# Performance work log

Measured on AMD Instinct MI355X. Metric: run time of the kernel, lower is better.

Reference implementation:

```python
import jax, jax.numpy as jnp
import numpy as np

EPS = 1e-08
SLOPE = 0.01  # LeakyReLU default negative_slope
B = 2097152
H = 32

def leaky_relu(x):
    return jnp.where(x >= 0, x, SLOPE * x)

def gram_schmidt(v, w):
    # v, w: [b,3]
    v_on = v / (jnp.linalg.norm(v, axis=-1, keepdims=True) + EPS)
    proj = jnp.sum(w * v_on, axis=-1, keepdims=True) * v_on
    w_orth = w - proj
    w_on = w_orth / (jnp.linalg.norm(w_orth, axis=-1, keepdims=True) + EPS)
    u_on = jnp.cross(v_on, w_on)
    R = jnp.stack((v_on, w_on, u_on), axis=-1)  # [b,3,3]
    v_local = jnp.einsum('bji,bj->bi', R, v)    # R^T @ v
    w_local = jnp.einsum('bji,bj->bi', R, w)
    return R, v_local, w_local

def setup_inputs() -> dict:
    key = jax.random.key(0)
    ks = jax.random.split(key, 12)
    std = 0.0001  # init_weights() normal std
    return {
        'v': jax.random.normal(ks[0], (B, 3), jnp.float32),
        'w': jax.random.normal(ks[1], (B, 3), jnp.float32),
        'W1': jax.random.normal(ks[2], (H, 3), jnp.float32) * std,
        'b1': jax.random.normal(ks[3], (H,), jnp.float32) * std,
        'W2': jax.random.normal(ks[4], (H, H), jnp.float32) * std,
        'b2': jax.random.normal(ks[5], (H,), jnp.float32) * std,
        'Wd1': jax.random.normal(ks[6], (H, H), jnp.float32) * std,
        'bd1': jax.random.normal(ks[7], (H,), jnp.float32) * std,
        'Wd2': jax.random.normal(ks[8], (3, H), jnp.float32) * std,
        'bd2': jax.random.normal(ks[9], (3,), jnp.float32) * std,
        'bias': jnp.array([[0.0, 0.0, -9.81]], jnp.float32),
    }

def reference(v, w, W1, b1, W2, b2, Wd1, bd1, Wd2, bd2, bias):
    shapes = v.shape
    b = shapes[0]
    v = v.reshape(b, 3)
    w = w.reshape(b, 3)
    R, v_local, w_local = gram_schmidt(v, w)
    feat = jnp.concatenate([v_local[..., :1], w_local[..., :2]], axis=-1)  # [b,3]
    h1 = leaky_relu(feat @ W1.T + b1)           # [b,H]
    h = leaky_relu(h1 @ W2.T + b2) * h1         # [b,H]
    y = leaky_relu(h @ Wd1.T + bd1) @ Wd2.T + bd2  # [b,3]
    y = jnp.einsum('bij,bj->bi', R, y) + bias
    return y.reshape(shapes)
```

## Files before the change

kernel.cpp:

```cpp
#include <hip/hip_runtime.h>

typedef __attribute__((ext_vector_type(8))) short short8;
typedef __attribute__((ext_vector_type(4))) float f32x4;
typedef __attribute__((ext_vector_type(2))) float f32x2;
typedef __attribute__((ext_vector_type(4))) unsigned int u32x4;

static __device__ __forceinline__ unsigned int fbits(float f) {
    union { float f; unsigned int u; } v; v.f = f; return v.u;
}
static __device__ __forceinline__ float bitsf(unsigned int u) {
    union { float f; unsigned int u; } v; v.u = u; return v.f;
}
static __device__ __forceinline__ unsigned int pkbf(float lo, float hi) {
    return __builtin_amdgcn_perm(fbits(hi), fbits(lo), 0x07060302u);
}
static __device__ __forceinline__ float bflo(unsigned int u) { return bitsf(u << 16); }
static __device__ __forceinline__ float bfhi(unsigned int u) { return bitsf(u & 0xFFFF0000u); }
static __device__ __forceinline__ float leaky(float x) { return fmaxf(x, 0.01f * x); }
static __device__ __forceinline__ float rsqrt_nr(float x) {
    const float r = __builtin_amdgcn_rsqf(x);
    return r * (1.5f - (0.5f * x) * (r * r));
}
static __device__ __forceinline__ f32x2 pk_mul_s(f32x2 s, f32x2 v) {
    f32x2 d; asm("v_pk_mul_f32 %0, %1, %2" : "=v"(d) : "s"(s), "v"(v)); return d;
}
static __device__ __forceinline__ f32x2 pk_fma_s(f32x2 s, f32x2 v, f32x2 c) {
    f32x2 d; asm("v_pk_fma_f32 %0, %1, %2, %3" : "=v"(d) : "s"(s), "v"(v), "v"(c)); return d;
}
static __device__ __forceinline__ f32x2 pk_add_s(f32x2 s, f32x2 v) {
    f32x2 d; asm("v_pk_add_f32 %0, %1, %2" : "=v"(d) : "s"(s), "v"(v)); return d;
}
static __device__ __forceinline__ f32x2 pk_mul_v(f32x2 a, f32x2 b) {
    f32x2 d; asm("v_pk_mul_f32 %0, %1, %2" : "=v"(d) : "v"(a), "v"(b)); return d;
}
static __device__ __forceinline__ f32x2 pk_fma_v(f32x2 a, f32x2 b, f32x2 c) {
    f32x2 d; asm("v_pk_fma_f32 %0, %1, %2, %3" : "=v"(d) : "v"(a), "v"(b), "v"(c)); return d;
}
static __device__ __forceinline__ f32x2 leaky2(f32x2 x, f32x2 c001) {
    const f32x2 m = pk_mul_v(x, c001);
    f32x2 r; r.x = fmaxf(x.x, m.x); r.y = fmaxf(x.y, m.y); return r;
}


__global__ __launch_bounds__(256, 4) void aero_mfma(
    const float* __restrict__ vin, const float* __restrict__ win,
    const float* __restrict__ gW1, const float* __restrict__ gb1,
    const float* __restrict__ gW2, const float* __restrict__ gb2,
    const float* __restrict__ gWd1, const float* __restrict__ gbd1,
    const float* __restrict__ gWd2, const float* __restrict__ gbd2,
    const float* __restrict__ gbias,
    float* __restrict__ out, int nrows)
{
    __shared__ unsigned int h1lds[256 * 20];

    const int tid  = threadIdx.x;
    int row = blockIdx.x * 256 + tid;
    if (row >= nrows) row = nrows - 1;

    const int i15   = tid & 15;
    const int quad  = (tid >> 4) & 3;
    const int wbase = tid & 192;
    const int ko    = 4 * quad;

    unsigned int aW2lo[4], aW2hi[4], aWd1lo[4], aWd1hi[4];
    {
        const float* p;
        p = gW2 + i15 * 32 + ko;
        { f32x4 xa = *(const f32x4*)p, xb = *(const f32x4*)(p + 16);
          #pragma unroll
          for (int j = 0; j < 4; ++j) aW2lo[j] = pkbf(xa[j], xb[j]); }
        p = gW2 + (16 + i15) * 32 + ko;
        { f32x4 xa = *(const f32x4*)p, xb = *(const f32x4*)(p + 16);
          #pragma unroll
          for (int j = 0; j < 4; ++j) aW2hi[j] = pkbf(xa[j], xb[j]); }
        p = gWd1 + i15 * 32 + ko;
        { f32x4 xa = *(const f32x4*)p, xb = *(const f32x4*)(p + 16);
          #pragma unroll
          for (int j = 0; j < 4; ++j) aWd1lo[j] = pkbf(xa[j], xb[j]); }
        p = gWd1 + (16 + i15) * 32 + ko;
        { f32x4 xa = *(const f32x4*)p, xb = *(const f32x4*)(p + 16);
          #pragma unroll
          for (int j = 0; j < 4; ++j) aWd1hi[j] = pkbf(xa[j], xb[j]); }
    }
    f32x2 wd2p[3][4];
    #pragma unroll
    for (int f = 0; f < 3; ++f) {
        const f32x4 xa = *(const f32x4*)(gWd2 + f * 32 + ko);
        const f32x4 xb = *(const f32x4*)(gWd2 + f * 32 + ko + 16);
        #pragma unroll
        for (int r = 0; r < 4; ++r) { wd2p[f][r].x = xa[r]; wd2p[f][r].y = xb[r]; }
    }
    const f32x4 cb2lo  = *(const f32x4*)(gb2  + ko);
    const f32x4 cb2hi  = *(const f32x4*)(gb2  + 16 + ko);
    const f32x4 cbd1lo = *(const f32x4*)(gbd1 + ko);
    const f32x4 cbd1hi = *(const f32x4*)(gbd1 + 16 + ko);

    const float v0 = vin[3 * row + 0], v1 = vin[3 * row + 1], v2 = vin[3 * row + 2];
    const float w0 = win[3 * row + 0], w1 = win[3 * row + 1], w2 = win[3 * row + 2];

    const float sv  = v0 * v0 + v1 * v1 + v2 * v2;
    const float rnv = rsqrt_nr(sv);
    const float a0 = v0 * rnv, a1 = v1 * rnv, a2 = v2 * rnv;
    const float proj = w0 * a0 + w1 * a1 + w2 * a2;
    const float o0 = w0 - proj * a0, o1 = w1 - proj * a1, o2 = w2 - proj * a2;
    const float sw  = o0 * o0 + o1 * o1 + o2 * o2;
    const float rnw = rsqrt_nr(sw);
    const float c0 = o0 * rnw, c1 = o1 * rnw, c2 = o2 * rnw;
    const float u0 = a1 * c2 - a2 * c1;
    const float u1 = a2 * c0 - a0 * c2;
    const float u2 = a0 * c1 - a1 * c0;

    const float f0 = sv * rnv, f1 = proj, f2 = sw * rnw;

    const f32x2 c001 = {0.01f, 0.01f};
    {
        const f32x2 fv0 = {f0, f0}, fv1 = {f1, f1}, fv2 = {f2, f2};
        unsigned int hp[16];
        #pragma unroll
        for (int j = 0; j < 16; ++j) {
            const f32x2 wp0 = {gW1[3 * j + 0], gW1[3 * (j + 16) + 0]};
            const f32x2 wp1 = {gW1[3 * j + 1], gW1[3 * (j + 16) + 1]};
            const f32x2 wp2 = {gW1[3 * j + 2], gW1[3 * (j + 16) + 2]};
            const f32x2 bb  = {gb1[j], gb1[j + 16]};
            f32x2 acc = pk_mul_s(wp0, fv0);
            acc = pk_fma_s(wp1, fv1, acc);
            acc = pk_fma_s(wp2, fv2, acc);
            acc = pk_add_s(bb, acc);
            const f32x2 h = leaky2(acc, c001);
            hp[j] = pkbf(h.x, h.y);
        }
        unsigned int* dst = &h1lds[tid * 20];
        *(u32x4*)(dst +  0) = (u32x4){hp[0],  hp[1],  hp[2],  hp[3]};
        *(u32x4*)(dst +  4) = (u32x4){hp[4],  hp[5],  hp[6],  hp[7]};
        *(u32x4*)(dst +  8) = (u32x4){hp[8],  hp[9],  hp[10], hp[11]};
        *(u32x4*)(dst + 12) = (u32x4){hp[12], hp[13], hp[14], hp[15]};
    }
    __syncthreads();

    float y0 = 0.f, y1 = 0.f, y2 = 0.f;
    #pragma unroll
    for (int t = 0; t < 4; ++t) {
        const u32x4 bfr = *(const u32x4*)(&h1lds[(wbase + 16 * t + i15) * 20 + ko]);
        const short8 bfrag = __builtin_bit_cast(short8, bfr);

        const f32x4 accA = __builtin_amdgcn_mfma_f32_16x16x32_bf16(
            __builtin_bit_cast(short8, (u32x4){aW2lo[0], aW2lo[1], aW2lo[2], aW2lo[3]}),
            bfrag, cb2lo, 0, 0, 0);
        const f32x4 accB = __builtin_amdgcn_mfma_f32_16x16x32_bf16(
            __builtin_bit_cast(short8, (u32x4){aW2hi[0], aW2hi[1], aW2hi[2], aW2hi[3]}),
            bfrag, cb2hi, 0, 0, 0);

        u32x4 h2u;
        #pragma unroll
        for (int r = 0; r < 4; ++r)
            h2u[r] = pkbf(leaky(accA[r]) * bflo(bfr[r]),
                          leaky(accB[r]) * bfhi(bfr[r]));
        const short8 h2frag = __builtin_bit_cast(short8, h2u);

        const f32x4 accC = __builtin_amdgcn_mfma_f32_16x16x32_bf16(
            __builtin_bit_cast(short8, (u32x4){aWd1lo[0], aWd1lo[1], aWd1lo[2], aWd1lo[3]}),
            h2frag, cbd1lo, 0, 0, 0);
        const f32x4 accD = __builtin_amdgcn_mfma_f32_16x16x32_bf16(
            __builtin_bit_cast(short8, (u32x4){aWd1hi[0], aWd1hi[1], aWd1hi[2], aWd1hi[3]}),
            h2frag, cbd1hi, 0, 0, 0);

        f32x2 h3p[4];
        #pragma unroll
        for (int r = 0; r < 4; ++r) { h3p[r].x = leaky(accC[r]); h3p[r].y = leaky(accD[r]); }
        f32x2 P0 = pk_mul_v(wd2p[0][0], h3p[0]);
        f32x2 P1 = pk_mul_v(wd2p[1][0], h3p[0]);
        f32x2 P2 = pk_mul_v(wd2p[2][0], h3p[0]);
        #pragma unroll
        for (int r = 1; r < 4; ++r) {
            P0 = pk_fma_v(wd2p[0][r], h3p[r], P0);
            P1 = pk_fma_v(wd2p[1][r], h3p[r], P1);
            P2 = pk_fma_v(wd2p[2][r], h3p[r], P2);
        }
        float s0 = P0.x + P0.y, s1 = P1.x + P1.y, s2 = P2.x + P2.y;
        s0 += __shfl_xor(s0, 16); s0 += __shfl_xor(s0, 32);
        s1 += __shfl_xor(s1, 16); s1 += __shfl_xor(s1, 32);
        s2 += __shfl_xor(s2, 16); s2 += __shfl_xor(s2, 32);
        if (quad == t) { y0 = s0; y1 = s1; y2 = s2; }
    }
    y0 += gbd2[0]; y1 += gbd2[1]; y2 += gbd2[2];

    out[3 * row + 0] = fmaf(a0, y0, fmaf(c0, y1, fmaf(u0, y2, gbias[0])));
    out[3 * row + 1] = fmaf(a1, y0, fmaf(c1, y1, fmaf(u1, y2, gbias[1])));
    out[3 * row + 2] = fmaf(a2, y0, fmaf(c2, y1, fmaf(u2, y2, gbias[2])));
}

extern "C" void kernel_launch(void* const* d_in, const int* in_sizes, int n_in,
                              void* d_out, int out_size, void* d_ws, size_t ws_size,
                              hipStream_t stream) {
    const float* v    = (const float*)d_in[0];
    const float* w    = (const float*)d_in[1];
    const float* W1   = (const float*)d_in[2];
    const float* b1   = (const float*)d_in[3];
    const float* W2   = (const float*)d_in[4];
    const float* b2   = (const float*)d_in[5];
    const float* Wd1  = (const float*)d_in[6];
    const float* bd1  = (const float*)d_in[7];
    const float* Wd2  = (const float*)d_in[8];
    const float* bd2  = (const float*)d_in[9];
    const float* bias = (const float*)d_in[10];

    const int nrows = in_sizes[0] / 3;
    dim3 block(256);
    dim3 grid((nrows + 255) / 256);
    hipLaunchKernelGGL(aero_mfma, grid, block, 0, stream,
                       v, w, W1, b1, W2, b2, Wd1, bd1, Wd2, bd2, bias,
                       (float*)d_out, nrows);
}
```

Baseline: 140.5 us.

## Process two rows per thread to amortize weight fragment setup

Each block now handles 512 rows with 256 threads, so each thread runs the Gram-Schmidt and first layer for two rows and then runs the MFMA chain twice. Per-thread weight loading, bf16 packing and constant setup are spread over twice as many rows, and the grid is halved. The cost is double the LDS per block and higher register pressure, which could reduce occupancy under the 4-block launch bound.

```diff
diff --git a/kernel.cpp b/kernel.cpp
--- a/kernel.cpp
+++ b/kernel.cpp
@@ -41,6 +41,96 @@
     f32x2 r; r.x = fmaxf(x.x, m.x); r.y = fmaxf(x.y, m.y); return r;
 }
 
+
+struct Rot { float a0,a1,a2,c0,c1,c2,u0,u1,u2; };
+
+static __device__ __forceinline__ Rot gs_l1(
+    const float* __restrict__ vin, const float* __restrict__ win,
+    const float* __restrict__ gW1, const float* __restrict__ gb1,
+    int row, unsigned int* __restrict__ dst)
+{
+    const float v0 = vin[3*row+0], v1 = vin[3*row+1], v2 = vin[3*row+2];
+    const float w0 = win[3*row+0], w1 = win[3*row+1], w2 = win[3*row+2];
+    const float sv  = v0*v0 + v1*v1 + v2*v2;
+    const float rnv = rsqrt_nr(sv);
+    const float a0 = v0*rnv, a1 = v1*rnv, a2 = v2*rnv;
+    const float proj = w0*a0 + w1*a1 + w2*a2;
+    const float o0 = w0 - proj*a0, o1 = w1 - proj*a1, o2 = w2 - proj*a2;
+    const float sw  = o0*o0 + o1*o1 + o2*o2;
+    const float rnw = rsqrt_nr(sw);
+    const float c0 = o0*rnw, c1 = o1*rnw, c2 = o2*rnw;
+    const float u0 = a1*c2 - a2*c1;
+    const float u1 = a2*c0 - a0*c2;
+    const float u2 = a0*c1 - a1*c0;
+    const float f0 = sv*rnv, f1 = proj, f2 = sw*rnw;
+
+    const f32x2 c001 = {0.01f, 0.01f};
+    const f32x2 fv0 = {f0,f0}, fv1 = {f1,f1}, fv2 = {f2,f2};
+    unsigned int hp[16];
+    #pragma unroll
+    for (int j = 0; j < 16; ++j) {
+        const f32x2 wp0 = {gW1[3*j+0], gW1[3*(j+16)+0]};
+        const f32x2 wp1 = {gW1[3*j+1], gW1[3*(j+16)+1]};
+        const f32x2 wp2 = {gW1[3*j+2], gW1[3*(j+16)+2]};
+        const f32x2 bb  = {gb1[j], gb1[j+16]};
+        f32x2 acc = pk_mul_s(wp0, fv0);
+        acc = pk_fma_s(wp1, fv1, acc);
+        acc = pk_fma_s(wp2, fv2, acc);
+        acc = pk_add_s(bb, acc);
+        const f32x2 h = leaky2(acc, c001);
+        hp[j] = pkbf(h.x, h.y);
+    }
+    *(u32x4*)(dst+0)  = (u32x4){hp[0],hp[1],hp[2],hp[3]};
+    *(u32x4*)(dst+4)  = (u32x4){hp[4],hp[5],hp[6],hp[7]};
+    *(u32x4*)(dst+8)  = (u32x4){hp[8],hp[9],hp[10],hp[11]};
+    *(u32x4*)(dst+12) = (u32x4){hp[12],hp[13],hp[14],hp[15]};
+    return {a0,a1,a2,c0,c1,c2,u0,u1,u2};
+}
+
+#define CHAIN234(LB, Y0, Y1, Y2)                                                   \
+    {                                                                              \
+        float s0k = 0.f, s1k = 0.f, s2k = 0.f;                                     \
+        _Pragma("unroll")                                                          \
+        for (int t = 0; t < 4; ++t) {                                              \
+            const u32x4 bfr = *(const u32x4*)(                                     \
+                &h1lds[((LB) + wbase + 16*t + i15)*20 + ko]);                      \
+            const short8 bfrag = __builtin_bit_cast(short8, bfr);                  \
+            const f32x4 accA = __builtin_amdgcn_mfma_f32_16x16x32_bf16(            \
+                fW2lo, bfrag, cb2lo, 0, 0, 0);                                     \
+            const f32x4 accB = __builtin_amdgcn_mfma_f32_16x16x32_bf16(            \
+                fW2hi, bfrag, cb2hi, 0, 0, 0);                                     \
+            u32x4 h2u;                                                             \
+            _Pragma("unroll")                                                      \
+            for (int r = 0; r < 4; ++r)                                            \
+                h2u[r] = pkbf(leaky(accA[r]) * bflo(bfr[r]),                       \
+                              leaky(accB[r]) * bfhi(bfr[r]));                      \
+            const short8 h2frag = __builtin_bit_cast(short8, h2u);                 \
+            const f32x4 accC = __builtin_amdgcn_mfma_f32_16x16x32_bf16(            \
+                fWd1lo, h2frag, cbd1lo, 0, 0, 0);                                  \
+            const f32x4 accD = __builtin_amdgcn_mfma_f32_16x16x32_bf16(            \
+                fWd1hi, h2frag, cbd1hi, 0, 0, 0);                                  \
+            f32x2 h30, h31, h32, h33;                                              \
+            h30.x = leaky(accC[0]); h30.y = leaky(accD[0]);                        \
+            h31.x = leaky(accC[1]); h31.y = leaky(accD[1]);                        \
+            h32.x = leaky(accC[2]); h32.y = leaky(accD[2]);                        \
+            h33.x = leaky(accC[3]); h33.y = leaky(accD[3]);                        \
+            f32x2 P0 = pk_mul_v(w00, h30);                                         \
+            f32x2 P1 = pk_mul_v(w10, h30);                                         \
+            f32x2 P2 = pk_mul_v(w20, h30);                                         \
+            P0 = pk_fma_v(w01, h31, P0); P1 = pk_fma_v(w11, h31, P1);              \
+            P2 = pk_fma_v(w21, h31, P2);                                           \
+            P0 = pk_fma_v(w02, h32, P0); P1 = pk_fma_v(w12, h32, P1);              \
+            P2 = pk_fma_v(w22, h32, P2);                                           \
+            P0 = pk_fma_v(w03, h33, P0); P1 = pk_fma_v(w13, h33, P1);              \
+            P2 = pk_fma_v(w23, h33, P2);                                           \
+            float s0 = P0.x + P0.y, s1 = P1.x + P1.y, s2 = P2.x + P2.y;            \
+            s0 += __shfl_xor(s0, 16); s0 += __shfl_xor(s0, 32);                    \
+            s1 += __shfl_xor(s1, 16); s1 += __shfl_xor(s1, 32);                    \
+            s2 += __shfl_xor(s2, 16); s2 += __shfl_xor(s2, 32);                    \
+            if (quad == t) { s0k = s0; s1k = s1; s2k = s2; }                       \
+        }                                                                          \
+        Y0 = s0k; Y1 = s1k; Y2 = s2k;                                              \
+    }
 
 __global__ __launch_bounds__(256, 4) void aero_mfma(
     const float* __restrict__ vin, const float* __restrict__ win,
@@ -51,17 +141,18 @@
     const float* __restrict__ gbias,
     float* __restrict__ out, int nrows)
 {
-    __shared__ unsigned int h1lds[256 * 20];
-
-    const int tid  = threadIdx.x;
-    int row = blockIdx.x * 256 + tid;
-    if (row >= nrows) row = nrows - 1;
-
+    __shared__ unsigned int h1lds[512 * 20];
+
+    const int tid   = threadIdx.x;
     const int i15   = tid & 15;
     const int quad  = (tid >> 4) & 3;
     const int wbase = tid & 192;
     const int ko    = 4 * quad;
 
+    const int base = blockIdx.x * 512;
+    int rowA = base + tid;        if (rowA >= nrows) rowA = nrows - 1;
+    int rowB = base + 256 + tid;  if (rowB >= nrows) rowB = nrows - 1;
+
     unsigned int aW2lo[4], aW2hi[4], aWd1lo[4], aWd1hi[4];
     {
         const float* p;
@@ -82,111 +173,49 @@
           #pragma unroll
           for (int j = 0; j < 4; ++j) aWd1hi[j] = pkbf(xa[j], xb[j]); }
     }
-    f32x2 wd2p[3][4];
-    #pragma unroll
-    for (int f = 0; f < 3; ++f) {
-        const f32x4 xa = *(const f32x4*)(gWd2 + f * 32 + ko);
-        const f32x4 xb = *(const f32x4*)(gWd2 + f * 32 + ko + 16);
-        #pragma unroll
-        for (int r = 0; r < 4; ++r) { wd2p[f][r].x = xa[r]; wd2p[f][r].y = xb[r]; }
+    const short8 fW2lo  = __builtin_bit_cast(short8, (u32x4){aW2lo[0],  aW2lo[1],  aW2lo[2],  aW2lo[3]});
+    const short8 fW2hi  = __builtin_bit_cast(short8, (u32x4){aW2hi[0],  aW2hi[1],  aW2hi[2],  aW2hi[3]});
+    const short8 fWd1lo = __builtin_bit_cast(short8, (u32x4){aWd1lo[0], aWd1lo[1], aWd1lo[2], aWd1lo[3]});
+    const short8 fWd1hi = __builtin_bit_cast(short8, (u32x4){aWd1hi[0], aWd1hi[1], aWd1hi[2], aWd1hi[3]});
+
+    f32x2 w00, w01, w02, w03, w10, w11, w12, w13, w20, w21, w22, w23;
+    {
+        f32x4 xa, xb;
+        xa = *(const f32x4*)(gWd2 + 0*32 + ko); xb = *(const f32x4*)(gWd2 + 0*32 + ko + 16);
+        w00.x = xa[0]; w00.y = xb[0]; w01.x = xa[1]; w01.y = xb[1];
+        w02.x = xa[2]; w02.y = xb[2]; w03.x = xa[3]; w03.y = xb[3];
+        xa = *(const f32x4*)(gWd2 + 1*32 + ko); xb = *(const f32x4*)(gWd2 + 1*32 + ko + 16);
+        w10.x = xa[0]; w10.y = xb[0]; w11.x = xa[1]; w11.y = xb[1];
+        w12.x = xa[2]; w12.y = xb[2]; w13.x = xa[3]; w13.y = xb[3];
+        xa = *(const f32x4*)(gWd2 + 2*32 + ko); xb = *(const f32x4*)(gWd2 + 2*32 + ko + 16);
+        w20.x = xa[0]; w20.y = xb[0]; w21.x = xa[1]; w21.y = xb[1];
+        w22.x = xa[2]; w22.y = xb[2]; w23.x = xa[3]; w23.y = xb[3];
     }
     const f32x4 cb2lo  = *(const f32x4*)(gb2  + ko);
     const f32x4 cb2hi  = *(const f32x4*)(gb2  + 16 + ko);
     const f32x4 cbd1lo = *(const f32x4*)(gbd1 + ko);
     const f32x4 cbd1hi = *(const f32x4*)(gbd1 + 16 + ko);
-
-    const float v0 = vin[3 * row + 0], v1 = vin[3 * row + 1], v2 = vin[3 * row + 2];
-    const float w0 = win[3 * row + 0], w1 = win[3 * row + 1], w2 = win[3 * row + 2];
-
-    const float sv  = v0 * v0 + v1 * v1 + v2 * v2;
-    const float rnv = rsqrt_nr(sv);
-    const float a0 = v0 * rnv, a1 = v1 * rnv, a2 = v2 * rnv;
-    const float proj = w0 * a0 + w1 * a1 + w2 * a2;
-    const float o0 = w0 - proj * a0, o1 = w1 - proj * a1, o2 = w2 - proj * a2;
-    const float sw  = o0 * o0 + o1 * o1 + o2 * o2;
-    const float rnw = rsqrt_nr(sw);
-    const float c0 = o0 * rnw, c1 = o1 * rnw, c2 = o2 * rnw;
-    const float u0 = a1 * c2 - a2 * c1;
-    const float u1 = a2 * c0 - a0 * c2;
-    const float u2 = a0 * c1 - a1 * c0;
-
-    const float f0 = sv * rnv, f1 = proj, f2 = sw * rnw;
-
-    const f32x2 c001 = {0.01f, 0.01f};
-    {
-        const f32x2 fv0 = {f0, f0}, fv1 = {f1, f1}, fv2 = {f2, f2};
-        unsigned int hp[16];
-        #pragma unroll
-        for (int j = 0; j < 16; ++j) {
-            const f32x2 wp0 = {gW1[3 * j + 0], gW1[3 * (j + 16) + 0]};
-            const f32x2 wp1 = {gW1[3 * j + 1], gW1[3 * (j + 16) + 1]};
-            const f32x2 wp2 = {gW1[3 * j + 2], gW1[3 * (j + 16) + 2]};
-            const f32x2 bb  = {gb1[j], gb1[j + 16]};
-            f32x2 acc = pk_mul_s(wp0, fv0);
-            acc = pk_fma_s(wp1, fv1, acc);
-            acc = pk_fma_s(wp2, fv2, acc);
-            acc = pk_add_s(bb, acc);
-            const f32x2 h = leaky2(acc, c001);
-            hp[j] = pkbf(h.x, h.y);
-        }
-        unsigned int* dst = &h1lds[tid * 20];
-        *(u32x4*)(dst +  0) = (u32x4){hp[0],  hp[1],  hp[2],  hp[3]};
-        *(u32x4*)(dst +  4) = (u32x4){hp[4],  hp[5],  hp[6],  hp[7]};
-        *(u32x4*)(dst +  8) = (u32x4){hp[8],  hp[9],  hp[10], hp[11]};
-        *(u32x4*)(dst + 12) = (u32x4){hp[12], hp[13], hp[14], hp[15]};
-    }
+    const f32x2 c001   = {0.01f, 0.01f};
+
+    const Rot RA = gs_l1(vin, win, gW1, gb1, rowA, &h1lds[tid * 20]);
+    const Rot RB = gs_l1(vin, win, gW1, gb1, rowB, &h1lds[(256 + tid) * 20]);
     __syncthreads();
 
-    float y0 = 0.f, y1 = 0.f, y2 = 0.f;
-    #pragma unroll
-    for (int t = 0; t < 4; ++t) {
-        const u32x4 bfr = *(const u32x4*)(&h1lds[(wbase + 16 * t + i15) * 20 + ko]);
-        const short8 bfrag = __builtin_bit_cast(short8, bfr);
-
-        const f32x4 accA = __builtin_amdgcn_mfma_f32_16x16x32_bf16(
-            __builtin_bit_cast(short8, (u32x4){aW2lo[0], aW2lo[1], aW2lo[2], aW2lo[3]}),
-            bfrag, cb2lo, 0, 0, 0);
-        const f32x4 accB = __builtin_amdgcn_mfma_f32_16x16x32_bf16(
-            __builtin_bit_cast(short8, (u32x4){aW2hi[0], aW2hi[1], aW2hi[2], aW2hi[3]}),
-            bfrag, cb2hi, 0, 0, 0);
-
-        u32x4 h2u;
-        #pragma unroll
-        for (int r = 0; r < 4; ++r)
-            h2u[r] = pkbf(leaky(accA[r]) * bflo(bfr[r]),
-                          leaky(accB[r]) * bfhi(bfr[r]));
-        const short8 h2frag = __builtin_bit_cast(short8, h2u);
-
-        const f32x4 accC = __builtin_amdgcn_mfma_f32_16x16x32_bf16(
-            __builtin_bit_cast(short8, (u32x4){aWd1lo[0], aWd1lo[1], aWd1lo[2], aWd1lo[3]}),
-            h2frag, cbd1lo, 0, 0, 0);
-        const f32x4 accD = __builtin_amdgcn_mfma_f32_16x16x32_bf16(
-            __builtin_bit_cast(short8, (u32x4){aWd1hi[0], aWd1hi[1], aWd1hi[2], aWd1hi[3]}),
-            h2frag, cbd1hi, 0, 0, 0);
-
-        f32x2 h3p[4];
-        #pragma unroll
-        for (int r = 0; r < 4; ++r) { h3p[r].x = leaky(accC[r]); h3p[r].y = leaky(accD[r]); }
-        f32x2 P0 = pk_mul_v(wd2p[0][0], h3p[0]);
-        f32x2 P1 = pk_mul_v(wd2p[1][0], h3p[0]);
-        f32x2 P2 = pk_mul_v(wd2p[2][0], h3p[0]);
-        #pragma unroll
-        for (int r = 1; r < 4; ++r) {
-            P0 = pk_fma_v(wd2p[0][r], h3p[r], P0);
-            P1 = pk_fma_v(wd2p[1][r], h3p[r], P1);
-            P2 = pk_fma_v(wd2p[2][r], h3p[r], P2);
-        }
-        float s0 = P0.x + P0.y, s1 = P1.x + P1.y, s2 = P2.x + P2.y;
-        s0 += __shfl_xor(s0, 16); s0 += __shfl_xor(s0, 32);
-        s1 += __shfl_xor(s1, 16); s1 += __shfl_xor(s1, 32);
-        s2 += __shfl_xor(s2, 16); s2 += __shfl_xor(s2, 32);
-        if (quad == t) { y0 = s0; y1 = s1; y2 = s2; }
-    }
-    y0 += gbd2[0]; y1 += gbd2[1]; y2 += gbd2[2];
-
-    out[3 * row + 0] = fmaf(a0, y0, fmaf(c0, y1, fmaf(u0, y2, gbias[0])));
-    out[3 * row + 1] = fmaf(a1, y0, fmaf(c1, y1, fmaf(u1, y2, gbias[1])));
-    out[3 * row + 2] = fmaf(a2, y0, fmaf(c2, y1, fmaf(u2, y2, gbias[2])));
+    float yA0, yA1, yA2, yB0, yB1, yB2;
+    CHAIN234(0,   yA0, yA1, yA2);
+    CHAIN234(256, yB0, yB1, yB2);
+
+    const float bd20 = gbd2[0], bd21 = gbd2[1], bd22 = gbd2[2];
+    const float gb0 = gbias[0], gb1v = gbias[1], gb2v = gbias[2];
+    yA0 += bd20; yA1 += bd21; yA2 += bd22;
+    yB0 += bd20; yB1 += bd21; yB2 += bd22;
+
+    out[3*rowA + 0] = fmaf(RA.a0, yA0, fmaf(RA.c0, yA1, fmaf(RA.u0, yA2, gb0)));
+    out[3*rowA + 1] = fmaf(RA.a1, yA0, fmaf(RA.c1, yA1, fmaf(RA.u1, yA2, gb1v)));
+    out[3*rowA + 2] = fmaf(RA.a2, yA0, fmaf(RA.c2, yA1, fmaf(RA.u2, yA2, gb2v)));
+    out[3*rowB + 0] = fmaf(RB.a0, yB0, fmaf(RB.c0, yB1, fmaf(RB.u0, yB2, gb0)));
+    out[3*rowB + 1] = fmaf(RB.a1, yB0, fmaf(RB.c1, yB1, fmaf(RB.u1, yB2, gb1v)));
+    out[3*rowB + 2] = fmaf(RB.a2, yB0, fmaf(RB.c2, yB1, fmaf(RB.u2, yB2, gb2v)));
 }
 
 extern "C" void kernel_launch(void* const* d_in, const int* in_sizes, int n_in,
@@ -206,7 +235,7 @@
 
     const int nrows = in_sizes[0] / 3;
     dim3 block(256);
-    dim3 grid((nrows + 255) / 256);
+    dim3 grid((nrows + 511) / 512);
     hipLaunchKernelGGL(aero_mfma, grid, block, 0, stream,
                        v, w, W1, b1, W2, b2, Wd1, bd1, Wd2, bd2, bias,
                        (float*)d_out, nrows);
```

Result: slower. 146.6 us (+4.3%).

## Compute first MLP layer with MFMA instead of per-thread packed FMAs

Applied to the files above, without the earlier changes.

Layer 1 (3->32) now runs as two bf16 MFMAs on a zero-padded feature fragment instead of per-thread packed-FP32 FMAs. Each thread writes only its three bf16 features to a smaller LDS buffer rather than 32 packed h1 values. This cuts per-thread VALU work and LDS traffic and lowers LDS footprint. The cost is two extra MFMAs per tile and bf16 rounding of the input features, which loses some precision.

```diff
diff --git a/kernel.cpp b/kernel.cpp
--- a/kernel.cpp
+++ b/kernel.cpp
@@ -14,31 +14,16 @@
 static __device__ __forceinline__ unsigned int pkbf(float lo, float hi) {
     return __builtin_amdgcn_perm(fbits(hi), fbits(lo), 0x07060302u);
 }
-static __device__ __forceinline__ float bflo(unsigned int u) { return bitsf(u << 16); }
-static __device__ __forceinline__ float bfhi(unsigned int u) { return bitsf(u & 0xFFFF0000u); }
 static __device__ __forceinline__ float leaky(float x) { return fmaxf(x, 0.01f * x); }
 static __device__ __forceinline__ float rsqrt_nr(float x) {
     const float r = __builtin_amdgcn_rsqf(x);
     return r * (1.5f - (0.5f * x) * (r * r));
-}
-static __device__ __forceinline__ f32x2 pk_mul_s(f32x2 s, f32x2 v) {
-    f32x2 d; asm("v_pk_mul_f32 %0, %1, %2" : "=v"(d) : "s"(s), "v"(v)); return d;
-}
-static __device__ __forceinline__ f32x2 pk_fma_s(f32x2 s, f32x2 v, f32x2 c) {
-    f32x2 d; asm("v_pk_fma_f32 %0, %1, %2, %3" : "=v"(d) : "s"(s), "v"(v), "v"(c)); return d;
-}
-static __device__ __forceinline__ f32x2 pk_add_s(f32x2 s, f32x2 v) {
-    f32x2 d; asm("v_pk_add_f32 %0, %1, %2" : "=v"(d) : "s"(s), "v"(v)); return d;
 }
 static __device__ __forceinline__ f32x2 pk_mul_v(f32x2 a, f32x2 b) {
     f32x2 d; asm("v_pk_mul_f32 %0, %1, %2" : "=v"(d) : "v"(a), "v"(b)); return d;
 }
 static __device__ __forceinline__ f32x2 pk_fma_v(f32x2 a, f32x2 b, f32x2 c) {
     f32x2 d; asm("v_pk_fma_f32 %0, %1, %2, %3" : "=v"(d) : "v"(a), "v"(b), "v"(c)); return d;
-}
-static __device__ __forceinline__ f32x2 leaky2(f32x2 x, f32x2 c001) {
-    const f32x2 m = pk_mul_v(x, c001);
-    f32x2 r; r.x = fmaxf(x.x, m.x); r.y = fmaxf(x.y, m.y); return r;
 }
 
 
@@ -51,131 +36,131 @@
     const float* __restrict__ gbias,
     float* __restrict__ out, int nrows)
 {
-    __shared__ unsigned int h1lds[256 * 20];
+    __shared__ unsigned int featlds[257 * 8];
 
-    const int tid  = threadIdx.x;
-    int row = blockIdx.x * 256 + tid;
-    if (row >= nrows) row = nrows - 1;
-
+    const int tid   = threadIdx.x;
     const int i15   = tid & 15;
     const int quad  = (tid >> 4) & 3;
     const int wbase = tid & 192;
     const int ko    = 4 * quad;
 
-    unsigned int aW2lo[4], aW2hi[4], aWd1lo[4], aWd1hi[4];
+    int row = blockIdx.x * 256 + tid;
+    if (row >= nrows) row = nrows - 1;
+
+    unsigned int a1lo[4] = {0,0,0,0}, a1hi[4] = {0,0,0,0};
+    if (quad == 0) {
+        #pragma unroll
+        for (int j = 0; j < 3; ++j) {
+            a1lo[j] = fbits(gW1[i15 * 3 + j]) >> 16;
+            a1hi[j] = fbits(gW1[(16 + i15) * 3 + j]) >> 16;
+        }
+    }
+    const short8 fW1lo = __builtin_bit_cast(short8, (u32x4){a1lo[0], a1lo[1], a1lo[2], a1lo[3]});
+    const short8 fW1hi = __builtin_bit_cast(short8, (u32x4){a1hi[0], a1hi[1], a1hi[2], a1hi[3]});
+
+    unsigned int a2lo[4], a2hi[4], a3lo[4], a3hi[4];
     {
         const float* p;
         p = gW2 + i15 * 32 + ko;
         { f32x4 xa = *(const f32x4*)p, xb = *(const f32x4*)(p + 16);
           #pragma unroll
-          for (int j = 0; j < 4; ++j) aW2lo[j] = pkbf(xa[j], xb[j]); }
+          for (int j = 0; j < 4; ++j) a2lo[j] = pkbf(xa[j], xb[j]); }
         p = gW2 + (16 + i15) * 32 + ko;
         { f32x4 xa = *(const f32x4*)p, xb = *(const f32x4*)(p + 16);
           #pragma unroll
-          for (int j = 0; j < 4; ++j) aW2hi[j] = pkbf(xa[j], xb[j]); }
+          for (int j = 0; j < 4; ++j) a2hi[j] = pkbf(xa[j], xb[j]); }
         p = gWd1 + i15 * 32 + ko;
         { f32x4 xa = *(const f32x4*)p, xb = *(const f32x4*)(p + 16);
           #pragma unroll
-          for (int j = 0; j < 4; ++j) aWd1lo[j] = pkbf(xa[j], xb[j]); }
+          for (int j = 0; j < 4; ++j) a3lo[j] = pkbf(xa[j], xb[j]); }
         p = gWd1 + (16 + i15) * 32 + ko;
         { f32x4 xa = *(const f32x4*)p, xb = *(const f32x4*)(p + 16);
           #pragma unroll
-          for (int j = 0; j < 4; ++j) aWd1hi[j] = pkbf(xa[j], xb[j]); }
+          for (int j = 0; j < 4; ++j) a3hi[j] = pkbf(xa[j], xb[j]); }
     }
-    f32x2 wd2p[3][4];
-    #pragma unroll
-    for (int f = 0; f < 3; ++f) {
-        const f32x4 xa = *(const f32x4*)(gWd2 + f * 32 + ko);
-        const f32x4 xb = *(const f32x4*)(gWd2 + f * 32 + ko + 16);
-        #pragma unroll
-        for (int r = 0; r < 4; ++r) { wd2p[f][r].x = xa[r]; wd2p[f][r].y = xb[r]; }
+    const short8 fW2lo  = __builtin_bit_cast(short8, (u32x4){a2lo[0], a2lo[1], a2lo[2], a2lo[3]});
+    const short8 fW2hi  = __builtin_bit_cast(short8, (u32x4){a2hi[0], a2hi[1], a2hi[2], a2hi[3]});
+    const short8 fWd1lo = __builtin_bit_cast(short8, (u32x4){a3lo[0], a3lo[1], a3lo[2], a3lo[3]});
+    const short8 fWd1hi = __builtin_bit_cast(short8, (u32x4){a3hi[0], a3hi[1], a3hi[2], a3hi[3]});
+
+    f32x2 w00, w01, w02, w03, w10, w11, w12, w13, w20, w21, w22, w23;
+    {
+        f32x4 xa, xb;
+        xa = *(const f32x4*)(gWd2 + 0*32 + ko); xb = *(const f32x4*)(gWd2 + 0*32 + ko + 16);
+        w00.x = xa[0]; w00.y = xb[0]; w01.x = xa[1]; w01.y = xb[1];
+        w02.x = xa[2]; w02.y = xb[2]; w03.x = xa[3]; w03.y = xb[3];
+        xa = *(const f32x4*)(gWd2 + 1*32 + ko); xb = *(const f32x4*)(gWd2 + 1*32 + ko + 16);
+        w10.x = xa[0]; w10.y = xb[0]; w11.x = xa[1]; w11.y = xb[1];
+        w12.x = xa[2]; w12.y = xb[2]; w13.x = xa[3]; w13.y = xb[3];
+        xa = *(const f32x4*)(gWd2 + 2*32 + ko); xb = *(const f32x4*)(gWd2 + 2*32 + ko + 16);
+        w20.x = xa[0]; w20.y = xb[0]; w21.x = xa[1]; w21.y = xb[1];
+        w22.x = xa[2]; w22.y = xb[2]; w23.x = xa[3]; w23.y = xb[3];
     }
+    const f32x4 cb1lo  = *(const f32x4*)(gb1  + ko);
+    const f32x4 cb1hi  = *(const f32x4*)(gb1  + 16 + ko);
     const f32x4 cb2lo  = *(const f32x4*)(gb2  + ko);
     const f32x4 cb2hi  = *(const f32x4*)(gb2  + 16 + ko);
     const f32x4 cbd1lo = *(const f32x4*)(gbd1 + ko);
     const f32x4 cbd1hi = *(const f32x4*)(gbd1 + 16 + ko);
 
-    const float v0 = vin[3 * row + 0], v1 = vin[3 * row + 1], v2 = vin[3 * row + 2];
-    const float w0 = win[3 * row + 0], w1 = win[3 * row + 1], w2 = win[3 * row + 2];
+    const float v0 = vin[3*row+0], v1 = vin[3*row+1], v2 = vin[3*row+2];
+    const float w0 = win[3*row+0], w1 = win[3*row+1], w2 = win[3*row+2];
 
-    const float sv  = v0 * v0 + v1 * v1 + v2 * v2;
+    const float sv  = v0*v0 + v1*v1 + v2*v2;
     const float rnv = rsqrt_nr(sv);
-    const float a0 = v0 * rnv, a1 = v1 * rnv, a2 = v2 * rnv;
-    const float proj = w0 * a0 + w1 * a1 + w2 * a2;
-    const float o0 = w0 - proj * a0, o1 = w1 - proj * a1, o2 = w2 - proj * a2;
-    const float sw  = o0 * o0 + o1 * o1 + o2 * o2;
+    const float a0 = v0*rnv, a1 = v1*rnv, a2 = v2*rnv;
+    const float proj = w0*a0 + w1*a1 + w2*a2;
+    const float o0 = w0 - proj*a0, o1 = w1 - proj*a1, o2 = w2 - proj*a2;
+    const float sw  = o0*o0 + o1*o1 + o2*o2;
     const float rnw = rsqrt_nr(sw);
-    const float c0 = o0 * rnw, c1 = o1 * rnw, c2 = o2 * rnw;
-    const float u0 = a1 * c2 - a2 * c1;
-    const float u1 = a2 * c0 - a0 * c2;
-    const float u2 = a0 * c1 - a1 * c0;
+    const float c0 = o0*rnw, c1 = o1*rnw, c2 = o2*rnw;
+    const float u0 = a1*c2 - a2*c1;
+    const float u1 = a2*c0 - a0*c2;
+    const float u2 = a0*c1 - a1*c0;
 
-    const float f0 = sv * rnv, f1 = proj, f2 = sw * rnw;
+    const float f0 = sv*rnv, f1 = proj, f2 = sw*rnw;
 
-    const f32x2 c001 = {0.01f, 0.01f};
-    {
-        const f32x2 fv0 = {f0, f0}, fv1 = {f1, f1}, fv2 = {f2, f2};
-        unsigned int hp[16];
-        #pragma unroll
-        for (int j = 0; j < 16; ++j) {
-            const f32x2 wp0 = {gW1[3 * j + 0], gW1[3 * (j + 16) + 0]};
-            const f32x2 wp1 = {gW1[3 * j + 1], gW1[3 * (j + 16) + 1]};
-            const f32x2 wp2 = {gW1[3 * j + 2], gW1[3 * (j + 16) + 2]};
-            const f32x2 bb  = {gb1[j], gb1[j + 16]};
-            f32x2 acc = pk_mul_s(wp0, fv0);
-            acc = pk_fma_s(wp1, fv1, acc);
-            acc = pk_fma_s(wp2, fv2, acc);
-            acc = pk_add_s(bb, acc);
-            const f32x2 h = leaky2(acc, c001);
-            hp[j] = pkbf(h.x, h.y);
-        }
-        unsigned int* dst = &h1lds[tid * 20];
-        *(u32x4*)(dst +  0) = (u32x4){hp[0],  hp[1],  hp[2],  hp[3]};
-        *(u32x4*)(dst +  4) = (u32x4){hp[4],  hp[5],  hp[6],  hp[7]};
-        *(u32x4*)(dst +  8) = (u32x4){hp[8],  hp[9],  hp[10], hp[11]};
-        *(u32x4*)(dst + 12) = (u32x4){hp[12], hp[13], hp[14], hp[15]};
-    }
+    *(u32x4*)(&featlds[tid * 8])     = (u32x4){ fbits(f0) >> 16, fbits(f1) >> 16,
+                                                fbits(f2) >> 16, 0u };
+    *(u32x4*)(&featlds[tid * 8 + 4]) = (u32x4){ 0u, 0u, 0u, 0u };
+    if (tid < 8) featlds[256 * 8 + tid] = 0u;
     __syncthreads();
 
     float y0 = 0.f, y1 = 0.f, y2 = 0.f;
     #pragma unroll
     for (int t = 0; t < 4; ++t) {
-        const u32x4 bfr = *(const u32x4*)(&h1lds[(wbase + 16 * t + i15) * 20 + ko]);
-        const short8 bfrag = __builtin_bit_cast(short8, bfr);
+        const u32x4 bfr = *(const u32x4*)(&featlds[(wbase + 16*t + i15) * 8 + ko]);
+        const short8 featfrag = __builtin_bit_cast(short8, bfr);
 
-        const f32x4 accA = __builtin_amdgcn_mfma_f32_16x16x32_bf16(
-            __builtin_bit_cast(short8, (u32x4){aW2lo[0], aW2lo[1], aW2lo[2], aW2lo[3]}),
-            bfrag, cb2lo, 0, 0, 0);
-        const f32x4 accB = __builtin_amdgcn_mfma_f32_16x16x32_bf16(
-            __builtin_bit_cast(short8, (u32x4){aW2hi[0], aW2hi[1], aW2hi[2], aW2hi[3]}),
-            bfrag, cb2hi, 0, 0, 0);
+        const f32x4 z1lo = __builtin_amdgcn_mfma_f32_16x16x32_bf16(fW1lo, featfrag, cb1lo, 0, 0, 0);
+        const f32x4 z1hi = __builtin_amdgcn_mfma_f32_16x16x32_bf16(fW1hi, featfrag, cb1hi, 0, 0, 0);
+        float h1l0 = leaky(z1lo[0]), h1l1 = leaky(z1lo[1]), h1l2 = leaky(z1lo[2]), h1l3 = leaky(z1lo[3]);
+        float h1h0 = leaky(z1hi[0]), h1h1 = leaky(z1hi[1]), h1h2 = leaky(z1hi[2]), h1h3 = leaky(z1hi[3]);
+        const short8 h1frag = __builtin_bit_cast(short8,
+            (u32x4){ pkbf(h1l0, h1h0), pkbf(h1l1, h1h1), pkbf(h1l2, h1h2), pkbf(h1l3, h1h3) });
 
-        u32x4 h2u;
-        #pragma unroll
-        for (int r = 0; r < 4; ++r)
-            h2u[r] = pkbf(leaky(accA[r]) * bflo(bfr[r]),
-                          leaky(accB[r]) * bfhi(bfr[r]));
-        const short8 h2frag = __builtin_bit_cast(short8, h2u);
+        const f32x4 z2lo = __builtin_amdgcn_mfma_f32_16x16x32_bf16(fW2lo, h1frag, cb2lo, 0, 0, 0);
+        const f32x4 z2hi = __builtin_amdgcn_mfma_f32_16x16x32_bf16(fW2hi, h1frag, cb2hi, 0, 0, 0);
+        const short8 h2frag = __builtin_bit_cast(short8, (u32x4){
+            pkbf(leaky(z2lo[0]) * h1l0, leaky(z2hi[0]) * h1h0),
+            pkbf(leaky(z2lo[1]) * h1l1, leaky(z2hi[1]) * h1h1),
+            pkbf(leaky(z2lo[2]) * h1l2, leaky(z2hi[2]) * h1h2),
+            pkbf(leaky(z2lo[3]) * h1l3, leaky(z2hi[3]) * h1h3) });
 
-        const f32x4 accC = __builtin_amdgcn_mfma_f32_16x16x32_bf16(
-            __builtin_bit_cast(short8, (u32x4){aWd1lo[0], aWd1lo[1], aWd1lo[2], aWd1lo[3]}),
-            h2frag, cbd1lo, 0, 0, 0);
-        const f32x4 accD = __builtin_amdgcn_mfma_f32_16x16x32_bf16(
-            __builtin_bit_cast(short8, (u32x4){aWd1hi[0], aWd1hi[1], aWd1hi[2], aWd1hi[3]}),
-            h2frag, cbd1hi, 0, 0, 0);
+        const f32x4 z3lo = __builtin_amdgcn_mfma_f32_16x16x32_bf16(fWd1lo, h2frag, cbd1lo, 0, 0, 0);
+        const f32x4 z3hi = __builtin_amdgcn_mfma_f32_16x16x32_bf16(fWd1hi, h2frag, cbd1hi, 0, 0, 0);
+        f32x2 h30, h31, h32, h33;
+        h30.x = leaky(z3lo[0]); h30.y = leaky(z3hi[0]);
+        h31.x = leaky(z3lo[1]); h31.y = leaky(z3hi[1]);
+        h32.x = leaky(z3lo[2]); h32.y = leaky(z3hi[2]);
+        h33.x = leaky(z3lo[3]); h33.y = leaky(z3hi[3]);
 
-        f32x2 h3p[4];
-        #pragma unroll
-        for (int r = 0; r < 4; ++r) { h3p[r].x = leaky(accC[r]); h3p[r].y = leaky(accD[r]); }
-        f32x2 P0 = pk_mul_v(wd2p[0][0], h3p[0]);
-        f32x2 P1 = pk_mul_v(wd2p[1][0], h3p[0]);
-        f32x2 P2 = pk_mul_v(wd2p[2][0], h3p[0]);
-        #pragma unroll
-        for (int r = 1; r < 4; ++r) {
-            P0 = pk_fma_v(wd2p[0][r], h3p[r], P0);
-            P1 = pk_fma_v(wd2p[1][r], h3p[r], P1);
-            P2 = pk_fma_v(wd2p[2][r], h3p[r], P2);
-        }
+        f32x2 P0 = pk_mul_v(w00, h30);
+        f32x2 P1 = pk_mul_v(w10, h30);
+        f32x2 P2 = pk_mul_v(w20, h30);
+        P0 = pk_fma_v(w01, h31, P0); P1 = pk_fma_v(w11, h31, P1); P2 = pk_fma_v(w21, h31, P2);
+        P0 = pk_fma_v(w02, h32, P0); P1 = pk_fma_v(w12, h32, P1); P2 = pk_fma_v(w22, h32, P2);
+        P0 = pk_fma_v(w03, h33, P0); P1 = pk_fma_v(w13, h33, P1); P2 = pk_fma_v(w23, h33, P2);
         float s0 = P0.x + P0.y, s1 = P1.x + P1.y, s2 = P2.x + P2.y;
         s0 += __shfl_xor(s0, 16); s0 += __shfl_xor(s0, 32);
         s1 += __shfl_xor(s1, 16); s1 += __shfl_xor(s1, 32);
@@ -184,9 +169,9 @@
     }
     y0 += gbd2[0]; y1 += gbd2[1]; y2 += gbd2[2];
 
-    out[3 * row + 0] = fmaf(a0, y0, fmaf(c0, y1, fmaf(u0, y2, gbias[0])));
-    out[3 * row + 1] = fmaf(a1, y0, fmaf(c1, y1, fmaf(u1, y2, gbias[1])));
-    out[3 * row + 2] = fmaf(a2, y0, fmaf(c2, y1, fmaf(u2, y2, gbias[2])));
+    out[3*row + 0] = fmaf(a0, y0, fmaf(c0, y1, fmaf(u0, y2, gbias[0])));
+    out[3*row + 1] = fmaf(a1, y0, fmaf(c1, y1, fmaf(u1, y2, gbias[1])));
+    out[3*row + 2] = fmaf(a2, y0, fmaf(c2, y1, fmaf(u2, y2, gbias[2])));
 }
 
 extern "C" void kernel_launch(void* const* d_in, const int* in_sizes, int n_in,
```

Result: slower. 147.1 us (+4.7%).
